# Performance work log

Hardware: AMD Instinct MI355X
Metric: run time of the kernel (lower is better)

## Reference

```python
import jax, jax.numpy as jnp
import numpy as np


def setup_inputs() -> dict:
    key = jax.random.key(0)
    k1, k2 = jax.random.split(key)
    B, N, M = 8, 8192, 8192
    preds = jax.random.normal(k1, (B, N, 3), dtype=jnp.float32)
    gts = jax.random.normal(k2, (B, M, 3), dtype=jnp.float32)
    return {"preds": preds, "gts": gts}


def _pairwise_sqdist(x, y):
    # x: [B, Nx, 3], y: [B, Ny, 3] -> P[b, i, j] = ||x_i - y_j||^2
    xx = jnp.sum(x * x, axis=-1)                      # [B, Nx]
    yy = jnp.sum(y * y, axis=-1)                      # [B, Ny]
    zz = jnp.einsum("bnd,bmd->bnm", x, y)            # [B, Nx, Ny]
    return xx[:, :, None] + yy[:, None, :] - 2.0 * zz


def reference(preds, gts):
    # matches forward with use_mask=False, reduce=False
    P = _pairwise_sqdist(gts, preds)                  # [B, M_gt, N_pred]
    loss_1 = jnp.mean(jnp.min(P, axis=1), axis=-1)    # min over gt points
    loss_2 = jnp.mean(jnp.min(P, axis=2), axis=-1)    # min over pred points
    return loss_1 + loss_2                            # [B]
```

## Files before the change

kernel.cpp:

```cpp
#include <hip/hip_runtime.h>

#define TPB 512
#define QPT 8
#define NCH (QPT / 2)
#define NSEG 32

typedef float v2f __attribute__((ext_vector_type(2)));

struct RefDup { double x2, y2, z2, w2; };

__device__ __forceinline__ unsigned encf(float f) {
    unsigned u = __float_as_uint(f);
    return (u & 0x80000000u) ? ~u : (u | 0x80000000u);
}
__device__ __forceinline__ float decf(unsigned u) {
    return __uint_as_float((u & 0x80000000u) ? (u ^ 0x80000000u) : ~u);
}
__device__ __forceinline__ double dup2(float v) {
    union { float f[2]; double d; } u; u.f[0] = v; u.f[1] = v; return u.d;
}

__device__ __forceinline__ v2f pk_fma_vs(v2f a, double b, v2f c) {
    v2f d; asm("v_pk_fma_f32 %0, %1, %2, %3" : "=v"(d) : "v"(a), "s"(b), "v"(c)); return d;
}

__global__ void __launch_bounds__(256) prep(const float* __restrict__ preds,
                                            const float* __restrict__ gts,
                                            RefDup* __restrict__ P8,
                                            RefDup* __restrict__ G8,
                                            unsigned* __restrict__ umins,
                                            int totalP, int totalG, int totalU) {
    int i = blockIdx.x * blockDim.x + threadIdx.x;
    if (i < totalP) {
        float x = preds[3 * i], y = preds[3 * i + 1], z = preds[3 * i + 2];
        RefDup r;
        r.x2 = dup2(x); r.y2 = dup2(y); r.z2 = dup2(z);
        r.w2 = dup2(fmaf(x, x, fmaf(y, y, z * z)));
        P8[i] = r;
    } else if (i < totalP + totalG) {
        int k = i - totalP;
        float x = gts[3 * k], y = gts[3 * k + 1], z = gts[3 * k + 2];
        RefDup r;
        r.x2 = dup2(x); r.y2 = dup2(y); r.z2 = dup2(z);
        r.w2 = dup2(fmaf(x, x, fmaf(y, y, z * z)));
        G8[k] = r;
    }
    if (i < totalU) umins[i] = 0xFFFFFFFFu;
}

__global__ void __launch_bounds__(TPB, 4) chamfer_dir(const RefDup* __restrict__ P8,
                                                      const RefDup* __restrict__ G8,
                                                      unsigned* __restrict__ umins,
                                                      int N, int M, int B, int nQpad) {
    const int db  = blockIdx.z;
    const int dir = db / B;
    const int b   = db - dir * B;
    const int seg = blockIdx.y;

    const RefDup* __restrict__ Qd = (dir == 0) ? (P8 + (size_t)b * N) : (G8 + (size_t)b * M);
    const RefDup* __restrict__ R  = (dir == 0) ? (G8 + (size_t)b * M) : (P8 + (size_t)b * N);
    const int nQ = (dir == 0) ? N : M;
    const int nR = (dir == 0) ? M : N;

    const int segLen = (nR + NSEG - 1) / NSEG;
    const int s0 = seg * segLen;
    const int s1 = (s0 + segLen < nR) ? (s0 + segLen) : nR;
    if (s0 >= s1) return;

    const int qbase = blockIdx.x * (TPB * QPT) + (int)threadIdx.x;

    v2f qx2[NCH], qy2[NCH], qz2[NCH], pw2[NCH], m2[NCH];
    #pragma unroll
    for (int c = 0; c < NCH; ++c) {
        const int qa = qbase + (2 * c) * TPB;
        const int qb = qbase + (2 * c + 1) * TPB;
        const int qac = (qa < nQ) ? qa : 0;
        const int qbc = (qb < nQ) ? qb : 0;
        const float* fa = (const float*)&Qd[qac];
        const float* fb = (const float*)&Qd[qbc];
        qx2[c].x = -2.f * fa[0]; qx2[c].y = -2.f * fb[0];
        qy2[c].x = -2.f * fa[2]; qy2[c].y = -2.f * fb[2];
        qz2[c].x = -2.f * fa[4]; qz2[c].y = -2.f * fb[4];
        pw2[c].x = fa[6];        pw2[c].y = fb[6];
        m2[c].x = 3.4e38f;       m2[c].y = 3.4e38f;
    }

    auto dupw = [](double w) -> v2f {
        union { double d; float f[2]; } u; u.d = w;
        v2f r; r.x = u.f[0]; r.y = u.f[1]; return r;
    };

    auto step4 = [&](const RefDup& r0, const RefDup& r1,
                     const RefDup& r2, const RefDup& r3) {
        v2f w0 = dupw(r0.w2), w1 = dupw(r1.w2), w2v = dupw(r2.w2), w3 = dupw(r3.w2);
        #pragma unroll
        for (int c = 0; c < NCH; ++c) {
            v2f d0 = pk_fma_vs(qz2[c], r0.z2, w0);
            d0 = pk_fma_vs(qy2[c], r0.y2, d0);
            d0 = pk_fma_vs(qx2[c], r0.x2, d0);
            v2f d1 = pk_fma_vs(qz2[c], r1.z2, w1);
            d1 = pk_fma_vs(qy2[c], r1.y2, d1);
            d1 = pk_fma_vs(qx2[c], r1.x2, d1);
            v2f d2 = pk_fma_vs(qz2[c], r2.z2, w2v);
            d2 = pk_fma_vs(qy2[c], r2.y2, d2);
            d2 = pk_fma_vs(qx2[c], r2.x2, d2);
            v2f d3 = pk_fma_vs(qz2[c], r3.z2, w3);
            d3 = pk_fma_vs(qy2[c], r3.y2, d3);
            d3 = pk_fma_vs(qx2[c], r3.x2, d3);
            m2[c].x = fminf(fminf(m2[c].x, d0.x), d1.x);
            m2[c].y = fminf(fminf(m2[c].y, d0.y), d1.y);
            m2[c].x = fminf(fminf(m2[c].x, d2.x), d3.x);
            m2[c].y = fminf(fminf(m2[c].y, d2.y), d3.y);
        }
    };

    int i = s0;
    if (s1 - s0 >= 8) {
        RefDup r0 = R[i], r1 = R[i + 1], r2 = R[i + 2], r3 = R[i + 3];
        for (; i + 8 <= s1; i += 4) {
            RefDup n0 = R[i + 4], n1 = R[i + 5], n2 = R[i + 6], n3 = R[i + 7];
            step4(r0, r1, r2, r3);
            r0 = n0; r1 = n1; r2 = n2; r3 = n3;
        }
        step4(r0, r1, r2, r3);
        i += 4;
    }
    for (; i < s1; ++i) {
        RefDup r = R[i];
        v2f wv = dupw(r.w2);
        #pragma unroll
        for (int c = 0; c < NCH; ++c) {
            v2f d = pk_fma_vs(qz2[c], r.z2, wv);
            d = pk_fma_vs(qy2[c], r.y2, d);
            d = pk_fma_vs(qx2[c], r.x2, d);
            m2[c].x = fminf(m2[c].x, d.x);
            m2[c].y = fminf(m2[c].y, d.y);
        }
    }

    unsigned* __restrict__ dst = umins + (size_t)db * nQpad;
    #pragma unroll
    for (int c = 0; c < NCH; ++c) {
        const int qa = qbase + (2 * c) * TPB;
        const int qb = qbase + (2 * c + 1) * TPB;
        if (qa < nQ) atomicMin(&dst[qa], encf(m2[c].x + pw2[c].x));
        if (qb < nQ) atomicMin(&dst[qb], encf(m2[c].y + pw2[c].y));
    }
}

__global__ void __launch_bounds__(256) finish(const unsigned* __restrict__ umins,
                                              float* __restrict__ out,
                                              int N, int M, int B, int nQpad) {
    const int b = blockIdx.x;
    const unsigned* m0 = umins + (size_t)b * nQpad;
    const unsigned* m1 = umins + (size_t)(B + b) * nQpad;

    float s0 = 0.f, s1 = 0.f;
    for (int q = (int)threadIdx.x; q < N; q += 256) s0 += decf(m0[q]);
    for (int q = (int)threadIdx.x; q < M; q += 256) s1 += decf(m1[q]);

    for (int off = 32; off > 0; off >>= 1) {
        s0 += __shfl_down(s0, off);
        s1 += __shfl_down(s1, off);
    }
    __shared__ float r0s[4], r1s[4];
    const int wid  = (int)threadIdx.x >> 6;
    const int lane = (int)threadIdx.x & 63;
    if (lane == 0) { r0s[wid] = s0; r1s[wid] = s1; }
    __syncthreads();
    if (threadIdx.x == 0) {
        float S0 = 0.f, S1 = 0.f;
        #pragma unroll
        for (int w = 0; w < 4; ++w) { S0 += r0s[w]; S1 += r1s[w]; }
        out[b] = S0 / (float)N + S1 / (float)M;
    }
}

extern "C" void kernel_launch(void* const* d_in, const int* in_sizes, int n_in,
                              void* d_out, int out_size, void* d_ws, size_t ws_size,
                              hipStream_t stream) {
    const float* preds = (const float*)d_in[0];
    const float* gts   = (const float*)d_in[1];
    float* out = (float*)d_out;

    const int B = out_size;
    const int N = in_sizes[0] / (B * 3);
    const int M = in_sizes[1] / (B * 3);
    const int nQpad = (N > M ? N : M);

    RefDup*   P8    = (RefDup*)d_ws;
    RefDup*   G8    = P8 + (size_t)B * N;
    unsigned* umins = (unsigned*)(G8 + (size_t)B * M);

    const int totalP = B * N;
    const int totalG = B * M;
    const int totalU = 2 * B * nQpad;
    const int prepTot = (totalP + totalG > totalU) ? (totalP + totalG) : totalU;
    prep<<<(prepTot + 255) / 256, 256, 0, stream>>>(preds, gts, P8, G8, umins,
                                                    totalP, totalG, totalU);

    const int qChunks = (nQpad + TPB * QPT - 1) / (TPB * QPT);
    dim3 grid(qChunks, NSEG, 2 * B);
    chamfer_dir<<<grid, TPB, 0, stream>>>(P8, G8, umins, N, M, B, nQpad);

    finish<<<B, 256, 0, stream>>>(umins, out, N, M, B, nQpad);
}
```

Baseline: 107.6 us.

## Stage reference points in LDS and use VGPR-operand packed FMAs

Reference points were read as wave-uniform scalar loads straight from global memory. Now each block cooperatively copies segments of up to 256 references into shared memory, and each lane reads them back as broadcast LDS loads into vector registers, double-buffered in quads of four. This removes the scalar-load latency and the s_waitcnt stalls on the SMEM path. In exchange it adds block barriers per segment, LDS read traffic and more VGPR pressure, which could reduce occupancy.

```diff
diff --git a/kernel.cpp b/kernel.cpp
--- a/kernel.cpp
+++ b/kernel.cpp
@@ -4,6 +4,7 @@
 #define QPT 8
 #define NCH (QPT / 2)
 #define NSEG 32
+#define SEGCAP 256
 
 typedef float v2f __attribute__((ext_vector_type(2)));
 
@@ -20,8 +21,8 @@
     union { float f[2]; double d; } u; u.f[0] = v; u.f[1] = v; return u.d;
 }
 
-__device__ __forceinline__ v2f pk_fma_vs(v2f a, double b, v2f c) {
-    v2f d; asm("v_pk_fma_f32 %0, %1, %2, %3" : "=v"(d) : "v"(a), "s"(b), "v"(c)); return d;
+__device__ __forceinline__ v2f pk_fma_vv(v2f a, v2f b, v2f c) {
+    v2f d; asm("v_pk_fma_f32 %0, %1, %2, %3" : "=v"(d) : "v"(a), "v"(b), "v"(c)); return d;
 }
 
 __global__ void __launch_bounds__(256) prep(const float* __restrict__ preds,
@@ -48,6 +49,18 @@
     if (i < totalU) umins[i] = 0xFFFFFFFFu;
 }
 
+struct Quad {
+    v2f x0, y0, z0, w0, x1, y1, z1, w1, x2, y2, z2, w2, x3, y3, z3, w3;
+};
+__device__ __forceinline__ Quad loadQuad(const v2f* __restrict__ L, int i) {
+    Quad q;
+    q.x0 = L[4 * i + 0];  q.y0 = L[4 * i + 1];  q.z0 = L[4 * i + 2];  q.w0 = L[4 * i + 3];
+    q.x1 = L[4 * i + 4];  q.y1 = L[4 * i + 5];  q.z1 = L[4 * i + 6];  q.w1 = L[4 * i + 7];
+    q.x2 = L[4 * i + 8];  q.y2 = L[4 * i + 9];  q.z2 = L[4 * i + 10]; q.w2 = L[4 * i + 11];
+    q.x3 = L[4 * i + 12]; q.y3 = L[4 * i + 13]; q.z3 = L[4 * i + 14]; q.w3 = L[4 * i + 15];
+    return q;
+}
+
 __global__ void __launch_bounds__(TPB, 4) chamfer_dir(const RefDup* __restrict__ P8,
                                                       const RefDup* __restrict__ G8,
                                                       unsigned* __restrict__ umins,
@@ -85,58 +98,66 @@
         m2[c].x = 3.4e38f;       m2[c].y = 3.4e38f;
     }
 
-    auto dupw = [](double w) -> v2f {
-        union { double d; float f[2]; } u; u.d = w;
-        v2f r; r.x = u.f[0]; r.y = u.f[1]; return r;
-    };
-
-    auto step4 = [&](const RefDup& r0, const RefDup& r1,
-                     const RefDup& r2, const RefDup& r3) {
-        v2f w0 = dupw(r0.w2), w1 = dupw(r1.w2), w2v = dupw(r2.w2), w3 = dupw(r3.w2);
-        #pragma unroll
-        for (int c = 0; c < NCH; ++c) {
-            v2f d0 = pk_fma_vs(qz2[c], r0.z2, w0);
-            d0 = pk_fma_vs(qy2[c], r0.y2, d0);
-            d0 = pk_fma_vs(qx2[c], r0.x2, d0);
-            v2f d1 = pk_fma_vs(qz2[c], r1.z2, w1);
-            d1 = pk_fma_vs(qy2[c], r1.y2, d1);
-            d1 = pk_fma_vs(qx2[c], r1.x2, d1);
-            v2f d2 = pk_fma_vs(qz2[c], r2.z2, w2v);
-            d2 = pk_fma_vs(qy2[c], r2.y2, d2);
-            d2 = pk_fma_vs(qx2[c], r2.x2, d2);
-            v2f d3 = pk_fma_vs(qz2[c], r3.z2, w3);
-            d3 = pk_fma_vs(qy2[c], r3.y2, d3);
-            d3 = pk_fma_vs(qx2[c], r3.x2, d3);
-            m2[c].x = fminf(fminf(m2[c].x, d0.x), d1.x);
-            m2[c].y = fminf(fminf(m2[c].y, d0.y), d1.y);
-            m2[c].x = fminf(fminf(m2[c].x, d2.x), d3.x);
-            m2[c].y = fminf(fminf(m2[c].y, d2.y), d3.y);
+    __shared__ float4 ldsbuf[SEGCAP * 2];
+    const v2f* __restrict__ L = (const v2f*)ldsbuf;
+
+#define CHAINS(q)                                                              \
+    do {                                                                       \
+        _Pragma("unroll")                                                      \
+        for (int c = 0; c < NCH; ++c) {                                        \
+            v2f d0 = pk_fma_vv(qz2[c], (q).z0, (q).w0);                        \
+            d0 = pk_fma_vv(qy2[c], (q).y0, d0);                                \
+            d0 = pk_fma_vv(qx2[c], (q).x0, d0);                                \
+            v2f d1 = pk_fma_vv(qz2[c], (q).z1, (q).w1);                        \
+            d1 = pk_fma_vv(qy2[c], (q).y1, d1);                                \
+            d1 = pk_fma_vv(qx2[c], (q).x1, d1);                                \
+            v2f d2 = pk_fma_vv(qz2[c], (q).z2, (q).w2);                        \
+            d2 = pk_fma_vv(qy2[c], (q).y2, d2);                                \
+            d2 = pk_fma_vv(qx2[c], (q).x2, d2);                                \
+            v2f d3 = pk_fma_vv(qz2[c], (q).z3, (q).w3);                        \
+            d3 = pk_fma_vv(qy2[c], (q).y3, d3);                                \
+            d3 = pk_fma_vv(qx2[c], (q).x3, d3);                                \
+            m2[c].x = fminf(fminf(m2[c].x, d0.x), d1.x);       \
+            m2[c].y = fminf(fminf(m2[c].y, d0.y), d1.y);                       \
+            m2[c].x = fminf(fminf(m2[c].x, d2.x), d3.x);                       \
+            m2[c].y = fminf(fminf(m2[c].y, d2.y), d3.y);                       \
+        }                                                                      \
+    } while (0)
+
+    for (int t0 = s0; t0 < s1; t0 += SEGCAP) {
+        const int t1 = (t0 + SEGCAP < s1) ? (t0 + SEGCAP) : s1;
+        const int len = t1 - t0;
+
+        __syncthreads();
+        const float4* __restrict__ Rv = (const float4*)(R + t0);
+        for (int t = (int)threadIdx.x; t < 2 * len; t += TPB) ldsbuf[t] = Rv[t];
+        __syncthreads();
+
+        int i = 0;
+        if (len >= 8) {
+            Quad A = loadQuad(L, 0);
+            Quad Bq = loadQuad(L, 4);
+            for (; i + 16 <= len; i += 8) {
+                CHAINS(A);  A  = loadQuad(L, i + 8);
+                CHAINS(Bq); Bq = loadQuad(L, i + 12);
+            }
+            CHAINS(A);
+            CHAINS(Bq);
+            i += 8;
         }
-    };
-
-    int i = s0;
-    if (s1 - s0 >= 8) {
-        RefDup r0 = R[i], r1 = R[i + 1], r2 = R[i + 2], r3 = R[i + 3];
-        for (; i + 8 <= s1; i += 4) {
-            RefDup n0 = R[i + 4], n1 = R[i + 5], n2 = R[i + 6], n3 = R[i + 7];
-            step4(r0, r1, r2, r3);
-            r0 = n0; r1 = n1; r2 = n2; r3 = n3;
+        for (; i < len; ++i) {
+            v2f rx = L[4 * i + 0], ry = L[4 * i + 1], rz = L[4 * i + 2], rw = L[4 * i + 3];
+            #pragma unroll
+            for (int c = 0; c < NCH; ++c) {
+                v2f d = pk_fma_vv(qz2[c], rz, rw);
+                d = pk_fma_vv(qy2[c], ry, d);
+                d = pk_fma_vv(qx2[c], rx, d);
+                m2[c].x = fminf(m2[c].x, d.x);
+                m2[c].y = fminf(m2[c].y, d.y);
+            }
         }
-        step4(r0, r1, r2, r3);
-        i += 4;
-    }
-    for (; i < s1; ++i) {
-        RefDup r = R[i];
-        v2f wv = dupw(r.w2);
-        #pragma unroll
-        for (int c = 0; c < NCH; ++c) {
-            v2f d = pk_fma_vs(qz2[c], r.z2, wv);
-            d = pk_fma_vs(qy2[c], r.y2, d);
-            d = pk_fma_vs(qx2[c], r.x2, d);
-            m2[c].x = fminf(m2[c].x, d.x);
-            m2[c].y = fminf(m2[c].y, d.y);
-        }
-    }
+    }
+#undef CHAINS
 
     unsigned* __restrict__ dst = umins + (size_t)db * nQpad;
     #pragma unroll
```

Result: slower. 126.0 us (+17.0%).
